# Optimization experiments

Measured on AMD Instinct MI355X. Metric: run time of the kernel, lower is better.

## Reference

```python
import jax, jax.numpy as jnp
import numpy as np

F = 20            # number of fields
V_FIELD = 5000    # vocab per field
TOTAL = F * V_FIELD
D = 64            # embedding dim (emd)
B = 8192          # batch
OFFSETS = jnp.arange(F, dtype=jnp.int32) * V_FIELD  # field offsets into shared table
_iu, _ju = np.triu_indices(F, k=1)                  # P = F*(F-1)/2 = 190 pairs
I_IDX = jnp.asarray(_iu, dtype=jnp.int32)
J_IDX = jnp.asarray(_ju, dtype=jnp.int32)


def setup_inputs() -> dict:
    key = jax.random.key(0)
    k1, k2, k3 = jax.random.split(key, 3)
    x = jax.random.randint(k1, (B, F), 0, V_FIELD, dtype=jnp.int32)
    # F field-aware embedding tables, each over the full offset vocab
    W = jax.random.normal(k2, (F, TOTAL, D), dtype=jnp.float32) * 0.01
    # linear term table (emd=1)
    Wl = jax.random.normal(k3, (TOTAL, 1), dtype=jnp.float32) * 0.01
    bias = jnp.zeros((1,), dtype=jnp.float32)
    return {"x": x, "W": W, "Wl": Wl, "bias": bias}


def reference(x, W, Wl, bias):
    idx = x + OFFSETS[None, :]                      # [B, F] global ids
    # embedding[:, j*F+i] == table j looked up at field-i's id
    a = W[J_IDX[None, :], idx[:, I_IDX]]            # [B, P, D] = V_j[x_i]
    b = W[I_IDX[None, :], idx[:, J_IDX]]            # [B, P, D] = V_i[x_j]
    interaction = jnp.sum(a * b, axis=(1, 2))[:, None]  # [B, 1]
    lin = Wl[idx].sum(axis=1)                       # [B, 1]
    return jax.nn.sigmoid(lin + bias + interaction)
```

## Files before the change

### kernel.cpp

```cpp
#include <hip/hip_runtime.h>
#include <math.h>


#define FF 20
#define V_FIELD 5000
#define TOTAL (FF * V_FIELD)
#define DD 64
#define SPB 4

__global__ __launch_bounds__(256) void ffm_kernel(
    const int* __restrict__ x,
    const float* __restrict__ W,
    const float* __restrict__ Wl,
    const float* __restrict__ bias,
    float* __restrict__ out)
{
    __shared__ int g[SPB][FF];
    const int t = threadIdx.x;
    const int sbase = blockIdx.x * SPB;

    if (t < SPB * FF) {
        const int s = t / FF, f = t % FF;
        g[s][f] = x[(sbase + s) * FF + f] + f * V_FIELD;
    }
    __syncthreads();

    const int wave = t >> 6;
    const int lane = t & 63;
    const int b = sbase + wave;

    int gi[FF];
#pragma unroll
    for (int i = 0; i < FF; ++i)
        gi[i] = __builtin_amdgcn_readfirstlane(g[wave][i]);

    float acc0 = 0.f, acc1 = 0.f, acc2 = 0.f, acc3 = 0.f;
    int p = 0;
#pragma unroll
    for (int i = 0; i < FF - 1; ++i) {
#pragma unroll
        for (int j = i + 1; j < FF; ++j) {
            const float a = W[((size_t)j * TOTAL + gi[i]) * DD + lane];
            const float c = W[((size_t)i * TOTAL + gi[j]) * DD + lane];
            switch (p & 3) {
                case 0: acc0 = fmaf(a, c, acc0); break;
                case 1: acc1 = fmaf(a, c, acc1); break;
                case 2: acc2 = fmaf(a, c, acc2); break;
                default: acc3 = fmaf(a, c, acc3); break;
            }
            ++p;
        }
    }
    float acc = (acc0 + acc1) + (acc2 + acc3);

    if (lane < FF) acc += Wl[g[wave][lane]];

#pragma unroll
    for (int off = 32; off > 0; off >>= 1)
        acc += __shfl_down(acc, off, 64);

    if (lane == 0)
        out[b] = 1.f / (1.f + expf(-(acc + bias[0])));
}

extern "C" void kernel_launch(void* const* d_in, const int* in_sizes, int n_in,
                              void* d_out, int out_size, void* d_ws, size_t ws_size,
                              hipStream_t stream) {
    const int*   x    = (const int*)d_in[0];
    const float* W    = (const float*)d_in[1];
    const float* Wl   = (const float*)d_in[2];
    const float* bias = (const float*)d_in[3];
    float* out = (float*)d_out;

    const int nB = out_size;
    dim3 grid(nB / SPB), block(256);
    hipLaunchKernelGGL(ffm_kernel, grid, block, 0, stream,
                       x, W, Wl, bias, out);
}
```

Baseline: 662.2 us.

## Gather embedding rows with float4 loads using precomputed per-pair LDS offsets

Precomputes the 190 field-pair (i,j) indices and per-sample byte offsets for both gathered rows into shared memory. Each wave then processes four pairs per iteration, with 16 lanes each loading a 256-byte row as float4 chunks. This replaces 380 scalar 4-byte loads per sample with far fewer wide loads and is meant to raise memory-level parallelism on the random gathers. It adds a setup phase, an extra barrier and LDS use, plus a launch-bounds occupancy hint.

New measurement: 661.4 us. About the same (-0.1%).

```diff
diff --git a/kernel.cpp b/kernel.cpp
--- a/kernel.cpp
+++ b/kernel.cpp
@@ -7,8 +7,10 @@
 #define TOTAL (FF * V_FIELD)
 #define DD 64
 #define SPB 4
+#define NP 190
+#define NPP 192
 
-__global__ __launch_bounds__(256) void ffm_kernel(
+__global__ __launch_bounds__(256, 4) void ffm_kernel(
     const int* __restrict__ x,
     const float* __restrict__ W,
     const float* __restrict__ Wl,
@@ -16,6 +18,9 @@
     float* __restrict__ out)
 {
     __shared__ int g[SPB][FF];
+    __shared__ short pi[NPP], pj[NPP];
+    __shared__ unsigned offA[SPB][NPP], offB[SPB][NPP];
+
     const int t = threadIdx.x;
     const int sbase = blockIdx.x * SPB;
 
@@ -23,35 +28,56 @@
         const int s = t / FF, f = t % FF;
         g[s][f] = x[(sbase + s) * FF + f] + f * V_FIELD;
     }
+    if (t < NPP) {
+        int pp = (t >= NP) ? 0 : t;
+        int i = 0;
+        while (pp >= FF - 1 - i) { pp -= FF - 1 - i; ++i; }
+        pi[t] = (short)i;
+        pj[t] = (short)(i + 1 + pp);
+    }
     __syncthreads();
 
     const int wave = t >> 6;
     const int lane = t & 63;
     const int b = sbase + wave;
 
-    int gi[FF];
-#pragma unroll
-    for (int i = 0; i < FF; ++i)
-        gi[i] = __builtin_amdgcn_readfirstlane(g[wave][i]);
-
-    float acc0 = 0.f, acc1 = 0.f, acc2 = 0.f, acc3 = 0.f;
-    int p = 0;
-#pragma unroll
-    for (int i = 0; i < FF - 1; ++i) {
-#pragma unroll
-        for (int j = i + 1; j < FF; ++j) {
-            const float a = W[((size_t)j * TOTAL + gi[i]) * DD + lane];
-            const float c = W[((size_t)i * TOTAL + gi[j]) * DD + lane];
-            switch (p & 3) {
-                case 0: acc0 = fmaf(a, c, acc0); break;
-                case 1: acc1 = fmaf(a, c, acc1); break;
-                case 2: acc2 = fmaf(a, c, acc2); break;
-                default: acc3 = fmaf(a, c, acc3); break;
-            }
-            ++p;
+    for (int q = lane; q < 2 * NPP; q += 64) {
+        if (q < NPP) {
+            const int p = q;
+            offA[wave][p] = (unsigned)(pj[p] * TOTAL + g[wave][pi[p]]) * (DD * 4);
+        } else {
+            const int p = q - NPP;
+            offB[wave][p] = (unsigned)(pi[p] * TOTAL + g[wave][pj[p]]) * (DD * 4);
         }
     }
-    float acc = (acc0 + acc1) + (acc2 + acc3);
+    __syncthreads();
+
+    const int grp = lane >> 4;
+    const unsigned chunk = (lane & 15) * 16;
+    const char* Wb = (const char*)W;
+
+    float a0 = 0.f, a1 = 0.f, a2 = 0.f, a3 = 0.f;
+
+#pragma unroll 4
+    for (int it = 0; it < 47; ++it) {
+        const int p = it * 4 + grp;
+        const float4 va = *(const float4*)(Wb + (offA[wave][p] + chunk));
+        const float4 vb = *(const float4*)(Wb + (offB[wave][p] + chunk));
+        a0 = fmaf(va.x, vb.x, a0);
+        a1 = fmaf(va.y, vb.y, a1);
+        a2 = fmaf(va.z, vb.z, a2);
+        a3 = fmaf(va.w, vb.w, a3);
+    }
+    if (grp < 2) {
+        const int p = 188 + grp;
+        const float4 va = *(const float4*)(Wb + (offA[wave][p] + chunk));
+        const float4 vb = *(const float4*)(Wb + (offB[wave][p] + chunk));
+        a0 = fmaf(va.x, vb.x, a0);
+        a1 = fmaf(va.y, vb.y, a1);
+        a2 = fmaf(va.z, vb.z, a2);
+        a3 = fmaf(va.w, vb.w, a3);
+    }
+    float acc = (a0 + a1) + (a2 + a3);
 
     if (lane < FF) acc += Wl[g[wave][lane]];
 
```

## Split FFM into pair-group work items with float4 loads and atomic accumulation

Applied to the files above, without the earlier changes.

Restructures the kernel so each block handles a group of four field pairs over a 256-sample chunk, not one sample per wave. The goal is to concentrate accesses to the same table slices within a block, improving cache locality for the 512MB W table, and to use 16-byte vector loads. Partial sums are combined with atomicAdd into a workspace, and a second kernel adds the linear term and applies the sigmoid. The cost is a memset, an extra launch and float atomics, which make the summation order nondeterministic.

New measurement: 691.3 us. 1.04x slower.

```diff
diff --git a/kernel.cpp b/kernel.cpp
--- a/kernel.cpp
+++ b/kernel.cpp
@@ -4,63 +4,98 @@
 
 #define FF 20
 #define V_FIELD 5000
-#define TOTAL (FF * V_FIELD)
+#define TOT (FF * V_FIELD)
 #define DD 64
-#define SPB 4
+#define NB 8192
+#define NP 190
+#define GPG 4
+#define NG 48
+#define SCH 256
+#define NCH (NB / SCH)
+#define NWORK (NG * NCH)
+#define GRID 512
 
-__global__ __launch_bounds__(256) void ffm_kernel(
+__global__ __launch_bounds__(256) void ffm_pairs(
     const int* __restrict__ x,
     const float* __restrict__ W,
+    float* __restrict__ acc)
+{
+    __shared__ short pi[GPG * NG], pj[GPG * NG];
+    __shared__ int gidx[SCH * FF];
+
+    const int t = threadIdx.x;
+
+    if (t < GPG * NG) {
+        int pp = (t >= NP) ? 0 : t;
+        int i = 0;
+        while (pp >= FF - 1 - i) { pp -= FF - 1 - i; ++i; }
+        pi[t] = (short)i;
+        pj[t] = (short)(i + 1 + pp);
+    }
+
+    const int wv   = t >> 6;
+    const int ln   = t & 63;
+    const int grp  = ln >> 4;
+    const int sub  = ln & 15;
+    const char* Wb = (const char*)W;
+
+    for (int w = blockIdx.x; w < NWORK; w += GRID) {
+        const int g_id  = w / NCH;
+        const int chunk = w % NCH;
+
+        __syncthreads();
+        for (int k = t; k < SCH * FF; k += 256) {
+            const int f = k % FF;
+            gidx[k] = x[chunk * (SCH * FF) + k] + f * V_FIELD;
+        }
+        __syncthreads();
+
+#pragma unroll 2
+        for (int q = 0; q < 16; ++q) {
+            const int sl = wv * 64 + q * 4 + grp;
+            float4 a4 = make_float4(0.f, 0.f, 0.f, 0.f);
+#pragma unroll
+            for (int k = 0; k < GPG; ++k) {
+                const int p = g_id * GPG + k;
+                if (p < NP) {
+                    const int i = pi[p], j = pj[p];
+                    const unsigned ga = (unsigned)gidx[sl * FF + i];
+                    const unsigned gb = (unsigned)gidx[sl * FF + j];
+                    const float4 va = *(const float4*)
+                        (Wb + (((unsigned)(j * TOT) + ga) << 8) + sub * 16);
+                    const float4 vb = *(const float4*)
+                        (Wb + (((unsigned)(i * TOT) + gb) << 8) + sub * 16);
+                    a4.x = fmaf(va.x, vb.x, a4.x);
+                    a4.y = fmaf(va.y, vb.y, a4.y);
+                    a4.z = fmaf(va.z, vb.z, a4.z);
+                    a4.w = fmaf(va.w, vb.w, a4.w);
+                }
+            }
+            float s = (a4.x + a4.y) + (a4.z + a4.w);
+            s += __shfl_xor(s, 1, 64);
+            s += __shfl_xor(s, 2, 64);
+            s += __shfl_xor(s, 4, 64);
+            s += __shfl_xor(s, 8, 64);
+            if (sub == 0)
+                atomicAdd(&acc[chunk * SCH + sl], s);
+        }
+    }
+}
+
+__global__ __launch_bounds__(256) void ffm_finish(
+    const int* __restrict__ x,
     const float* __restrict__ Wl,
     const float* __restrict__ bias,
+    const float* __restrict__ acc,
     float* __restrict__ out)
 {
-    __shared__ int g[SPB][FF];
-    const int t = threadIdx.x;
-    const int sbase = blockIdx.x * SPB;
-
-    if (t < SPB * FF) {
-        const int s = t / FF, f = t % FF;
-        g[s][f] = x[(sbase + s) * FF + f] + f * V_FIELD;
-    }
-    __syncthreads();
-
-    const int wave = t >> 6;
-    const int lane = t & 63;
-    const int b = sbase + wave;
-
-    int gi[FF];
+    const int b = blockIdx.x * 256 + threadIdx.x;
+    float s = acc[b];
+    const int* xr = x + b * FF;
 #pragma unroll
-    for (int i = 0; i < FF; ++i)
-        gi[i] = __builtin_amdgcn_readfirstlane(g[wave][i]);
-
-    float acc0 = 0.f, acc1 = 0.f, acc2 = 0.f, acc3 = 0.f;
-    int p = 0;
-#pragma unroll
-    for (int i = 0; i < FF - 1; ++i) {
-#pragma unroll
-        for (int j = i + 1; j < FF; ++j) {
-            const float a = W[((size_t)j * TOTAL + gi[i]) * DD + lane];
-            const float c = W[((size_t)i * TOTAL + gi[j]) * DD + lane];
-            switch (p & 3) {
-                case 0: acc0 = fmaf(a, c, acc0); break;
-                case 1: acc1 = fmaf(a, c, acc1); break;
-                case 2: acc2 = fmaf(a, c, acc2); break;
-                default: acc3 = fmaf(a, c, acc3); break;
-            }
-            ++p;
-        }
-    }
-    float acc = (acc0 + acc1) + (acc2 + acc3);
-
-    if (lane < FF) acc += Wl[g[wave][lane]];
-
-#pragma unroll
-    for (int off = 32; off > 0; off >>= 1)
-        acc += __shfl_down(acc, off, 64);
-
-    if (lane == 0)
-        out[b] = 1.f / (1.f + expf(-(acc + bias[0])));
+    for (int f = 0; f < FF; ++f)
+        s += Wl[xr[f] + f * V_FIELD];
+    out[b] = 1.f / (1.f + expf(-(s + bias[0])));
 }
 
 extern "C" void kernel_launch(void* const* d_in, const int* in_sizes, int n_in,
@@ -71,9 +106,10 @@
     const float* Wl   = (const float*)d_in[2];
     const float* bias = (const float*)d_in[3];
     float* out = (float*)d_out;
+    float* acc = (float*)d_ws;
 
-    const int nB = out_size;
-    dim3 grid(nB / SPB), block(256);
-    hipLaunchKernelGGL(ffm_kernel, grid, block, 0, stream,
-                       x, W, Wl, bias, out);
+    hipMemsetAsync(acc, 0, NB * sizeof(float), stream);
+    hipLaunchKernelGGL(ffm_pairs, dim3(GRID), dim3(256), 0, stream, x, W, acc);
+    hipLaunchKernelGGL(ffm_finish, dim3(NB / 256), dim3(256), 0, stream,
+                       x, Wl, bias, acc, out);
 }
```
